# Kernel tuning notes

Measured on AMD Instinct MI355X. Metric: run time of the kernel, lower is better.

The kernel has to match this reference:

```python
import jax, jax.numpy as jnp
import numpy as np

B, S, H = 64, 256, 1024

def setup_inputs() -> dict:
    key = jax.random.key(0)
    ks = jax.random.split(key, 9)
    sc = 1.0 / np.sqrt(H)
    return {
        "x":     jax.random.normal(ks[0], (B, S, H), dtype=jnp.float32),
        "h0":    jax.random.normal(ks[1], (B, H), dtype=jnp.float32) * 0.1,
        "c0":    jax.random.normal(ks[2], (B, H), dtype=jnp.float32) * 0.1,
        "Wx":    jax.random.normal(ks[3], (4, H, H), dtype=jnp.float32) * sc,   # gates i,f,c,o: input 1x1-conv weights
        "bx":    jax.random.normal(ks[4], (4, H), dtype=jnp.float32) * 0.01,
        "Wh":    jax.random.normal(ks[5], (4, H, H), dtype=jnp.float32) * sc,   # gates i,f,c,o: hidden 1x1-conv weights
        "bh":    jax.random.normal(ks[6], (4, H), dtype=jnp.float32) * 0.01,
        "peep":  jax.random.normal(ks[7], (3, H), dtype=jnp.float32) * 0.1,     # peephole W_i, W_f, W_o
        "bgate": jax.random.normal(ks[8], (4, H), dtype=jnp.float32) * 0.1,     # b_i, b_f, b_c, b_o
    }

def reference(x, h0, c0, Wx, bx, Wh, bh, peep, bgate):
    # ConvNorm with kernel_size=1 is a matmul over the channel (hidden) dim.
    # Input-side gate pre-activations have no recurrence: precompute for all steps.
    # xg: (S, 4, B, H)
    xg = jnp.einsum('bsh,gkh->sgbk', x, Wx) + bx[None, :, None, :]

    def step(carry, xt):
        h, c = carry                                   # (B,H) each
        hg = jnp.einsum('bh,gkh->gbk', h, Wh) + bh[:, None, :]   # (4,B,H)
        i_g = jax.nn.sigmoid(xt[0] + hg[0] + peep[0] * c + bgate[0])
        f_g = jax.nn.sigmoid(xt[1] + hg[1] + peep[1] * c + bgate[1])
        # NOTE: original code adds ingate (ct = f*c + i + tanh(...)), not i*tanh.
        c_n = f_g * c + i_g + jnp.tanh(xt[2] + hg[2] + bgate[2])
        o_g = jax.nn.sigmoid(xt[3] + hg[3] + peep[2] * c_n + bgate[3])
        h_n = o_g * jnp.tanh(c_n)
        return (h_n, c_n), h_n

    (_, _), hs = jax.lax.scan(step, (h0, c0), xg)      # hs: (S,B,H)
    return jnp.transpose(hs, (1, 0, 2))                # batch_first output (B,S,H)
```

## Files before the change

### kernel.cpp

```cpp
#include <hip/hip_runtime.h>


#define S_LEN 256
#define H_DIM 1024
#define B_DIM 64
#define SENT 0x7FFF7FFFu
#define XROW 1042

typedef _Float16 v8h __attribute__((ext_vector_type(8)));
typedef float v4f __attribute__((ext_vector_type(4)));
typedef unsigned v4u __attribute__((ext_vector_type(4)));

__device__ __forceinline__ v8h pack8h(float4 a, float4 b) {
  v8h r;
  r[0] = (_Float16)a.x; r[1] = (_Float16)a.y; r[2] = (_Float16)a.z; r[3] = (_Float16)a.w;
  r[4] = (_Float16)b.x; r[5] = (_Float16)b.y; r[6] = (_Float16)b.z; r[7] = (_Float16)b.w;
  return r;
}

__device__ __forceinline__ float fsigmoid(float x) { return 1.0f / (1.0f + __expf(-x)); }
__device__ __forceinline__ float ftanh(float x) {
  float e = __expf(2.0f * x);
  return 1.0f - 2.0f / (e + 1.0f);
}

__global__ void k_init(unsigned* __restrict__ hb) {
  int i = blockIdx.x * 256 + threadIdx.x;
  for (int idx = i; idx < 4 * B_DIM * H_DIM / 2; idx += gridDim.x * 256)
    hb[idx] = SENT;
}

__global__ __launch_bounds__(256, 1) void lstm_fused(
    const float* __restrict__ x, const float* __restrict__ Wx,
    const float* __restrict__ Wh, const float* __restrict__ h0,
    const float* __restrict__ c0, const float* __restrict__ bx,
    const float* __restrict__ bh, const float* __restrict__ bgate,
    const float* __restrict__ peep, float* __restrict__ out,
    _Float16* __restrict__ hbuf) {
  __shared__ float pre[4][4][16][18];
  __shared__ _Float16 ldsx[2][16 * XROW];
  __shared__ _Float16 hstage[16][16];

  const int tid = threadIdx.x;
  const int wid = tid >> 6;
  const int lane = tid & 63;
  const int la = lane & 15;
  const int lq = lane >> 4;
  const int cluster = blockIdx.x >> 6;
  const int slot = blockIdx.x & 63;
  const int ch0 = slot * 16;
  const int b0 = cluster * 16;

  v8h wh_f[4][8], wx_f[4][8];
  {
    const int col = wid * 256 + lq * 8;
#pragma unroll
    for (int g = 0; g < 4; ++g) {
#pragma unroll
      for (int kk = 0; kk < 8; ++kk) {
        const float* ph = Wh + (size_t)(g * 1024 + ch0 + la) * 1024 + col + kk * 32;
        wh_f[g][kk] = pack8h(*(const float4*)ph, *(const float4*)(ph + 4));
        const float* px = Wx + (size_t)(g * 1024 + ch0 + la) * 1024 + col + kk * 32;
        wx_f[g][kk] = pack8h(*(const float4*)px, *(const float4*)(px + 4));
      }
    }
  }

  const int bl = tid >> 4;
  const int nn = tid & 15;
  const int gb = b0 + bl;
  const int ch = ch0 + nn;
  float bias_c[4];
#pragma unroll
  for (int g = 0; g < 4; ++g)
    bias_c[g] = bx[g * 1024 + ch] + bh[g * 1024 + ch] + bgate[g * 1024 + ch];
  const float pI = peep[ch], pF = peep[1024 + ch], pO = peep[2048 + ch];
  float c_st = c0[gb * 1024 + ch];

  float4 sreg[16];
  auto stage_load = [&](int ts) {
#pragma unroll
    for (int j = 0; j < 8; ++j) {
      int cid = tid + j * 256;
      int row = cid >> 7, c8 = cid & 127;
      const float* px = x + (size_t)(b0 + row) * (S_LEN * H_DIM) + (size_t)ts * H_DIM + c8 * 8;
      sreg[2 * j] = *(const float4*)px;
      sreg[2 * j + 1] = *(const float4*)(px + 4);
    }
  };
  auto stage_write = [&](int buf) {
#pragma unroll
    for (int j = 0; j < 8; ++j) {
      int cid = tid + j * 256;
      int row = cid >> 7, c8 = cid & 127;
      *(v8h*)(&ldsx[buf][row * XROW + c8 * 8]) = pack8h(sreg[2 * j], sreg[2 * j + 1]);
    }
  };
  const v4f vzero = {0.f, 0.f, 0.f, 0.f};
  v4f acc[4];
  auto xmfma = [&](int buf) {
#pragma unroll
    for (int kk = 0; kk < 8; ++kk) {
      v8h ax = *(const v8h*)(&ldsx[buf][la * XROW + wid * 256 + kk * 32 + lq * 8]);
#pragma unroll
      for (int g = 0; g < 4; ++g)
        acc[g] = __builtin_amdgcn_mfma_f32_16x16x32_f16(ax, wx_f[g][kk], acc[g], 0, 0, 0);
    }
  };

  stage_load(0); stage_write(0);
  __syncthreads();
#pragma unroll
  for (int g = 0; g < 4; ++g) acc[g] = vzero;
  xmfma(0);
  stage_load(1); stage_write(1);

  for (int t = 0; t < S_LEN; ++t) {
    v8h ah[8];
    if (t == 0) {
      const float* hrow = h0 + (size_t)(b0 + la) * H_DIM + wid * 256 + lq * 8;
#pragma unroll
      for (int kk = 0; kk < 8; ++kk)
        ah[kk] = pack8h(*(const float4*)(hrow + kk * 32),
                        *(const float4*)(hrow + kk * 32 + 4));
    } else {
      const _Float16* hb = hbuf + ((t - 1) & 3) * (B_DIM * H_DIM) +
                           (size_t)(b0 + la) * H_DIM + wid * 256 + lq * 8;
      v4u u0, u1, u2, u3, u4, u5, u6, u7;
      for (;;) {
        asm volatile(
            "global_load_dwordx4 %0, %[p], off sc0 sc1\n\t"
            "global_load_dwordx4 %1, %[p], off offset:64 sc0 sc1\n\t"
            "global_load_dwordx4 %2, %[p], off offset:128 sc0 sc1\n\t"
            "global_load_dwordx4 %3, %[p], off offset:192 sc0 sc1\n\t"
            "global_load_dwordx4 %4, %[p], off offset:256 sc0 sc1\n\t"
            "global_load_dwordx4 %5, %[p], off offset:320 sc0 sc1\n\t"
            "global_load_dwordx4 %6, %[p], off offset:384 sc0 sc1\n\t"
            "global_load_dwordx4 %7, %[p], off offset:448 sc0 sc1\n\t"
            "s_waitcnt vmcnt(0)"
            : "=&v"(u0), "=&v"(u1), "=&v"(u2), "=&v"(u3),
              "=&v"(u4), "=&v"(u5), "=&v"(u6), "=&v"(u7)
            : [p] "v"(hb)
            : "memory");
        int ok = (u0[0] != SENT) & (u0[1] != SENT) & (u0[2] != SENT) & (u0[3] != SENT) &
                 (u1[0] != SENT) & (u1[1] != SENT) & (u1[2] != SENT) & (u1[3] != SENT) &
                 (u2[0] != SENT) & (u2[1] != SENT) & (u2[2] != SENT) & (u2[3] != SENT) &
                 (u3[0] != SENT) & (u3[1] != SENT) & (u3[2] != SENT) & (u3[3] != SENT) &
                 (u4[0] != SENT) & (u4[1] != SENT) & (u4[2] != SENT) & (u4[3] != SENT) &
                 (u5[0] != SENT) & (u5[1] != SENT) & (u5[2] != SENT) & (u5[3] != SENT) &
                 (u6[0] != SENT) & (u6[1] != SENT) & (u6[2] != SENT) & (u6[3] != SENT) &
                 (u7[0] != SENT) & (u7[1] != SENT) & (u7[2] != SENT) & (u7[3] != SENT);
        if (__all(ok)) break;
        __builtin_amdgcn_s_sleep(1);
      }
      ah[0] = __builtin_bit_cast(v8h, u0); ah[1] = __builtin_bit_cast(v8h, u1);
      ah[2] = __builtin_bit_cast(v8h, u2); ah[3] = __builtin_bit_cast(v8h, u3);
      ah[4] = __builtin_bit_cast(v8h, u4); ah[5] = __builtin_bit_cast(v8h, u5);
      ah[6] = __builtin_bit_cast(v8h, u6); ah[7] = __builtin_bit_cast(v8h, u7);
    }
#pragma unroll
    for (int kk = 0; kk < 8; ++kk) {
#pragma unroll
      for (int g = 0; g < 4; ++g)
        acc[g] = __builtin_amdgcn_mfma_f32_16x16x32_f16(ah[kk], wh_f[g][kk], acc[g], 0, 0, 0);
    }

#pragma unroll
    for (int g = 0; g < 4; ++g)
#pragma unroll
      for (int r = 0; r < 4; ++r)
        pre[wid][g][lq * 4 + r][la] = acc[g][r];
    __syncthreads();

    if (t < S_LEN - 2) stage_load(t + 2);

    float s[4];
#pragma unroll
    for (int g = 0; g < 4; ++g)
      s[g] = pre[0][g][bl][nn] + pre[1][g][bl][nn] + pre[2][g][bl][nn] +
             pre[3][g][bl][nn] + bias_c[g];
    float ig = fsigmoid(s[0] + pI * c_st);
    float fg = fsigmoid(s[1] + pF * c_st);
    float cn = fg * c_st + ig + ftanh(s[2]);
    float og = fsigmoid(s[3] + pO * cn);
    float hn = og * ftanh(cn);
    c_st = cn;

    hstage[bl][nn] = (_Float16)hn;
    out[((size_t)gb * S_LEN + t) * H_DIM + ch] = hn;
    __syncthreads();

    if (t < S_LEN - 1) {
      if (tid < 32) {
        const int b = tid >> 1, half = tid & 1;
        v4u d = *(const v4u*)(&hstage[b][half * 8]);
        _Float16* hp = hbuf + (t & 3) * (B_DIM * H_DIM) +
                       (size_t)(b0 + b) * H_DIM + ch0 + half * 8;
        asm volatile("global_store_dwordx4 %[p], %[d], off sc0 sc1"
                     :: [p] "v"(hp), [d] "v"(d) : "memory");
        if (t >= 2) {
          v4u sv = {SENT, SENT, SENT, SENT};
          _Float16* rp = hbuf + ((t - 2) & 3) * (B_DIM * H_DIM) +
                         (size_t)(b0 + b) * H_DIM + ch0 + half * 8;
          asm volatile("global_store_dwordx4 %[p], %[d], off sc0 sc1"
                       :: [p] "v"(rp), [d] "v"(sv) : "memory");
        }
      }
#pragma unroll
      for (int g = 0; g < 4; ++g) acc[g] = vzero;
      xmfma((t + 1) & 1);
      if (t < S_LEN - 2) stage_write(t & 1);
    }
  }
}

extern "C" void kernel_launch(void* const* d_in, const int* in_sizes, int n_in,
                              void* d_out, int out_size, void* d_ws, size_t ws_size,
                              hipStream_t stream) {
  (void)in_sizes; (void)n_in; (void)out_size; (void)ws_size;
  const float* x    = (const float*)d_in[0];
  const float* h0   = (const float*)d_in[1];
  const float* c0   = (const float*)d_in[2];
  const float* Wx   = (const float*)d_in[3];
  const float* bx   = (const float*)d_in[4];
  const float* Wh   = (const float*)d_in[5];
  const float* bh   = (const float*)d_in[6];
  const float* peep = (const float*)d_in[7];
  const float* bg   = (const float*)d_in[8];
  float* out = (float*)d_out;

  _Float16* hbuf = (_Float16*)d_ws;

  k_init<<<64, 256, 0, stream>>>((unsigned*)d_ws);
  lstm_fused<<<256, 256, 0, stream>>>(x, Wx, Wh, h0, c0, bx, bh, bg, peep,
                                      out, hbuf);
}
```

Baseline: 1.190 ms.

## Add per-block progress flags to gate hidden-state polling before bulk loads

Adds a small array of per-block step counters. Each producer block writes its counter after storing its h slice, and consumers spin on cheap single-dword flag loads before issuing the eight-wide hidden-state loads. The sentinel reset store is moved after the input MFMA work so it no longer sits on the critical publish path, and the spin sleep durations are raised. The aim is to cut memory traffic and contention from repeated wide polling across 256 blocks. The cost is an extra flag round-trip of latency per step. The flag store has no explicit fence against the data stores, so correctness still relies on the sentinel check.

After: 1.277 ms. +7.3%, slower.

```diff
diff --git a/kernel.cpp b/kernel.cpp
--- a/kernel.cpp
+++ b/kernel.cpp
@@ -24,10 +24,11 @@
   return 1.0f - 2.0f / (e + 1.0f);
 }
 
-__global__ void k_init(unsigned* __restrict__ hb) {
+__global__ void k_init(unsigned* __restrict__ hb, unsigned* __restrict__ hints) {
   int i = blockIdx.x * 256 + threadIdx.x;
   for (int idx = i; idx < 4 * B_DIM * H_DIM / 2; idx += gridDim.x * 256)
     hb[idx] = SENT;
+  if (i < 256) hints[i] = 0u;
 }
 
 __global__ __launch_bounds__(256, 1) void lstm_fused(
@@ -36,7 +37,7 @@
     const float* __restrict__ c0, const float* __restrict__ bx,
     const float* __restrict__ bh, const float* __restrict__ bgate,
     const float* __restrict__ peep, float* __restrict__ out,
-    _Float16* __restrict__ hbuf) {
+    _Float16* __restrict__ hbuf, unsigned* __restrict__ hints) {
   __shared__ float pre[4][4][16][18];
   __shared__ _Float16 ldsx[2][16 * XROW];
   __shared__ _Float16 hstage[16][16];
@@ -124,6 +125,19 @@
         ah[kk] = pack8h(*(const float4*)(hrow + kk * 32),
                         *(const float4*)(hrow + kk * 32 + 4));
     } else {
+      {
+        const unsigned* hintp = hints + cluster * 64 + wid * 16 + la;
+        const unsigned tgt = (unsigned)t;
+        unsigned hv;
+        for (;;) {
+          asm volatile(
+              "global_load_dword %0, %[p], off sc0 sc1\n\t"
+              "s_waitcnt vmcnt(0)"
+              : "=v"(hv) : [p] "v"(hintp) : "memory");
+          if (__all((int)(hv >= tgt))) break;
+          __builtin_amdgcn_s_sleep(8);
+        }
+      }
       const _Float16* hb = hbuf + ((t - 1) & 3) * (B_DIM * H_DIM) +
                            (size_t)(b0 + la) * H_DIM + wid * 256 + lq * 8;
       v4u u0, u1, u2, u3, u4, u5, u6, u7;
@@ -151,7 +165,7 @@
                  (u6[0] != SENT) & (u6[1] != SENT) & (u6[2] != SENT) & (u6[3] != SENT) &
                  (u7[0] != SENT) & (u7[1] != SENT) & (u7[2] != SENT) & (u7[3] != SENT);
         if (__all(ok)) break;
-        __builtin_amdgcn_s_sleep(1);
+        __builtin_amdgcn_s_sleep(2);
       }
       ah[0] = __builtin_bit_cast(v8h, u0); ah[1] = __builtin_bit_cast(v8h, u1);
       ah[2] = __builtin_bit_cast(v8h, u2); ah[3] = __builtin_bit_cast(v8h, u3);
@@ -198,18 +212,25 @@
                        (size_t)(b0 + b) * H_DIM + ch0 + half * 8;
         asm volatile("global_store_dwordx4 %[p], %[d], off sc0 sc1"
                      :: [p] "v"(hp), [d] "v"(d) : "memory");
-        if (t >= 2) {
-          v4u sv = {SENT, SENT, SENT, SENT};
-          _Float16* rp = hbuf + ((t - 2) & 3) * (B_DIM * H_DIM) +
-                         (size_t)(b0 + b) * H_DIM + ch0 + half * 8;
-          asm volatile("global_store_dwordx4 %[p], %[d], off sc0 sc1"
-                       :: [p] "v"(rp), [d] "v"(sv) : "memory");
-        }
+      }
+      if (tid == 0) {
+        unsigned tag = (unsigned)(t + 1);
+        unsigned* hq = hints + cluster * 64 + slot;
+        asm volatile("global_store_dword %[p], %[d], off sc0 sc1"
+                     :: [p] "v"(hq), [d] "v"(tag) : "memory");
       }
 #pragma unroll
       for (int g = 0; g < 4; ++g) acc[g] = vzero;
       xmfma((t + 1) & 1);
       if (t < S_LEN - 2) stage_write(t & 1);
+      if (tid < 32 && t >= 2) {
+        const int b = tid >> 1, half = tid & 1;
+        v4u sv = {SENT, SENT, SENT, SENT};
+        _Float16* rp = hbuf + ((t - 2) & 3) * (B_DIM * H_DIM) +
+                       (size_t)(b0 + b) * H_DIM + ch0 + half * 8;
+        asm volatile("global_store_dwordx4 %[p], %[d], off sc0 sc1"
+                     :: [p] "v"(rp), [d] "v"(sv) : "memory");
+      }
     }
   }
 }
@@ -230,8 +251,9 @@
   float* out = (float*)d_out;
 
   _Float16* hbuf = (_Float16*)d_ws;
-
-  k_init<<<64, 256, 0, stream>>>((unsigned*)d_ws);
+  unsigned* hints = (unsigned*)((char*)d_ws + 4 * B_DIM * H_DIM * 2);
+
+  k_init<<<64, 256, 0, stream>>>((unsigned*)d_ws, hints);
   lstm_fused<<<256, 256, 0, stream>>>(x, Wx, Wh, h0, c0, bx, bh, bg, peep,
-                                      out, hbuf);
-}
+                                      out, hbuf, hints);
+}
```
